# Kernel tuning notes

Measured on AMD Instinct MI355X. Metric: run time of the kernel, lower is better.

Reference implementation:

```python
import jax, jax.numpy as jnp
import numpy as np

B, C, CK, CV, W, H = 8, 256, 256, 256, 64, 64
EPS = 1e-6

def setup_inputs() -> dict:
    key = jax.random.key(0)
    ks = jax.random.split(key, 13)
    def wmat(k, shape, fan_in):
        return jax.random.normal(k, shape, jnp.float32) / np.float32(np.sqrt(fan_in))
    return {
        "x": jax.random.normal(ks[0], (B, C, W, H), jnp.float32),
        "qw": wmat(ks[1], (CK, C), C), "qb": jnp.zeros((CK,), jnp.float32),
        "kw": wmat(ks[2], (CK, C), C), "kb": jnp.zeros((CK,), jnp.float32),
        "vw": wmat(ks[3], (CV, C), C), "vb": jnp.zeros((CV,), jnp.float32),
        "rw": wmat(ks[4], (C, CV), CV), "rb": jnp.zeros((C,), jnp.float32),
        "c1w": wmat(ks[5], (C, C, 3, 3), C * 9), "c1b": jnp.zeros((C,), jnp.float32),
        "c2w": wmat(ks[6], (C, C, 3, 3), C * 9), "c2b": jnp.zeros((C,), jnp.float32),
    }

def reference(x, qw, qb, kw, kb, vw, vb, rw, rb, c1w, c1b, c2w, c2b):
    Bz, Cc, Wd, Hd = x.shape
    n = Wd * Hd
    xf = x.reshape(Bz, Cc, n)                                  # [b,c,n]
    Q = jnp.einsum('oc,bcn->bon', qw, xf) + qb[None, :, None]  # 1x1 conv
    K = jnp.einsum('oc,bcn->bon', kw, xf) + kb[None, :, None]
    V = jnp.einsum('oc,bcn->bon', vw, xf) + vb[None, :, None]
    # l2 norm over channel dim (per token), exactly as torch.norm(dim=-2)
    Qn = Q / jnp.linalg.norm(Q, axis=1, keepdims=True)
    Kn = K / jnp.linalg.norm(K, axis=1, keepdims=True)
    Qt = jnp.transpose(Qn, (0, 2, 1))                          # [b,n,ck]
    # head loops in the original sum over the full channel dim -> single einsum
    agg_dom = jnp.einsum('bnk,bk->bn', Qt, Kn.sum(-1))         # [b,n]
    denom = 1.0 / (n + agg_dom + EPS)                          # [b,n]
    vsum = V.sum(-1)                                           # [b,cv]
    kv = jnp.einsum('bkn,bcn->bkc', Kn, V)                     # K^T V, [b,ck,cv]
    qkv = jnp.einsum('bnk,bkc->bcn', Qt, kv)                   # [b,cv,n]
    wv = (vsum[:, :, None] + qkv) * denom[:, None, :]
    wv = wv.reshape(Bz, -1, Hd, Wd)                            # matches torch .view(b,cv,h,w)
    attn = jnp.einsum('oc,bchw->bohw', rw, wv) + rb[None, :, None, None]
    dn = ('NCHW', 'OIHW', 'NCHW')
    h = jax.lax.conv_general_dilated(attn, c1w, (1, 1), 'SAME', dimension_numbers=dn) + c1b[None, :, None, None]
    h = jax.lax.conv_general_dilated(h, c2w, (1, 1), 'SAME', dimension_numbers=dn) + c2b[None, :, None, None]
    return h * x + x
```

## Files before the change

### kernel.cpp

```cpp
#include <hip/hip_runtime.h>
#include <math.h>


typedef unsigned short u16;
typedef __attribute__((ext_vector_type(8))) short short8;
typedef __attribute__((ext_vector_type(4))) float f32x4;
typedef __attribute__((ext_vector_type(4))) unsigned short us4v;

#define ASYNC16(g, l) __builtin_amdgcn_global_load_lds( \
    (const __attribute__((address_space(1))) unsigned int*)(g), \
    (__attribute__((address_space(3))) unsigned int*)(l), 16, 0, 0)

static __device__ __forceinline__ float b2f(u16 h) {
  unsigned int u = ((unsigned int)h) << 16;
  return __builtin_bit_cast(float, u);
}
static __device__ __forceinline__ u16 f2b(float f) {
  unsigned int u = __builtin_bit_cast(unsigned int, f);
  u += 0x7fffu + ((u >> 16) & 1u);
  return (u16)(u >> 16);
}

#define NB 1048576L

__global__ __launch_bounds__(256) void prep1(
    const float* __restrict__ qw, const float* __restrict__ kw,
    const float* __restrict__ vw, const float* __restrict__ rw,
    const float* __restrict__ c1w, const float* __restrict__ c2w,
    const float* __restrict__ kb, const float* __restrict__ vb,
    const float* __restrict__ rb,
    u16* __restrict__ qw16, u16* __restrict__ kvw16, u16* __restrict__ rwT16,
    u16* __restrict__ wr1, u16* __restrict__ wr2,
    float* __restrict__ kvbias, float* __restrict__ zbuf, float* __restrict__ T)
{
  if (blockIdx.x >= 5633) {
    int m = blockIdx.x - 5633, co = threadIdx.x;
    float r = rb[co];
    const float* p = c1w + (long)m * 2304 + co * 9;
    float lv[9];
#pragma unroll
    for (int d = 0; d < 9; d++) lv[d] = p[d] * r;
#pragma unroll
    for (int d = 0; d < 9; d++)
#pragma unroll
      for (int off = 32; off; off >>= 1) lv[d] += __shfl_down(lv[d], off, 64);
    __shared__ float red[4][9];
    int w = co >> 6, l = co & 63;
    if (l == 0)
#pragma unroll
      for (int d = 0; d < 9; d++) red[w][d] = lv[d];
    __syncthreads();
    if (co < 9) T[m * 9 + co] = red[0][co] + red[1][co] + red[2][co] + red[3][co];
    return;
  }
  if (blockIdx.x == 5632) {
    int t = threadIdx.x;
    if (t < 256) { kvbias[t] = kb[t]; kvbias[t + 256] = vb[t]; }
    if (t < 64) zbuf[t] = 0.f;
    return;
  }
  long g = (long)blockIdx.x * 256 + threadIdx.x;
  if (g < 65536) {
    qw16[g] = f2b(qw[g]);
  } else if (g < 196608) {
    long e = g - 65536;
    kvw16[e] = f2b(e < 65536 ? kw[e] : vw[e - 65536]);
  } else if (g < 262144) {
    long e = g - 196608;
    int cv = e >> 8, co = e & 255;
    rwT16[e] = f2b(rw[co * 256 + cv]);
  } else if (g < 851968) {
    long e = g - 262144;
    int m = e / 2304, r = e - m * 2304;
    int d = r >> 8, c = r & 255;
    wr1[e] = f2b(c1w[m * 2304 + c * 9 + d]);
  } else {
    long e = g - 851968;
    int m = e / 2304, r = e - m * 2304;
    int d = r >> 8, c = r & 255;
    wr2[e] = f2b(c2w[m * 2304 + c * 9 + d]);
  }
}

__global__ __launch_bounds__(256) void transX(
    const float* __restrict__ x, u16* __restrict__ xT)
{
  __shared__ float Tl[64][65];
  int lin = blockIdx.x, t = threadIdx.x;
  int n0 = (lin & 63) * 64, c0 = ((lin >> 6) & 3) * 64, b = lin >> 8;
#pragma unroll
  for (int i = 0; i < 4; i++) {
    int c = (t >> 4) + i * 16, nn = (t & 15) * 4;
    float4 v = *(const float4*)&x[(long)b * NB + (long)(c0 + c) * 4096 + n0 + nn];
    Tl[c][nn] = v.x; Tl[c][nn + 1] = v.y; Tl[c][nn + 2] = v.z; Tl[c][nn + 3] = v.w;
  }
  __syncthreads();
#pragma unroll
  for (int i = 0; i < 4; i++) {
    int n = (t >> 4) + i * 16, cc = (t & 15) * 4;
    us4v o;
#pragma unroll
    for (int e = 0; e < 4; e++) o[e] = f2b(Tl[cc + e][n]);
    *(us4v*)&xT[(long)b * NB + (long)(n0 + n) * 256 + c0 + cc] = o;
  }
}

__global__ __launch_bounds__(256) void gemm3(
    const u16* __restrict__ wr1, const u16* __restrict__ rwT16, u16* __restrict__ w1p,
    const u16* __restrict__ xT, const u16* __restrict__ qw16, u16* __restrict__ Qt,
    const u16* __restrict__ kvw16, u16* __restrict__ KV,
    const float* __restrict__ qb, const float* __restrict__ kvbias,
    const float* __restrict__ T, const float* __restrict__ c1b,
    float* __restrict__ corr)
{
  __shared__ __align__(16) u16 As[2][128 * 32];
  __shared__ __align__(16) u16 Bs[2][128 * 32];
  int lin = blockIdx.x;
  if (lin >= 1572) {
    int e = (lin - 1572) * 256 + threadIdx.x;
    int m = e & 255, p = e >> 8;
    int y = p >> 6, xx = p & 63;
    float s = c1b[m];
#pragma unroll
    for (int d = 0; d < 9; d++) {
      int dy = d / 3 - 1, dx = d - (d / 3) * 3 - 1;
      if ((unsigned)(y + dy) < 64u && (unsigned)(xx + dx) < 64u) s += T[m * 9 + d];
    }
    corr[e] = s;
    return;
  }
  const u16 *A, *B;
  u16* out;
  const float *p1, *p2;
  long i0, j0, aoff, boff, ooff, sR;
  if (lin < 36) {
    int bx = lin & 1, by = lin >> 1;
    A = wr1; B = rwT16; out = w1p;
    i0 = by * 128; j0 = bx * 128;
    aoff = 0; boff = 0; ooff = 0; sR = 256;
    p1 = nullptr; p2 = nullptr;
  } else if (lin < 548) {
    int e = lin - 36;
    int bx = e & 1, by = (e >> 1) & 31, b = e >> 6;
    A = xT; B = qw16; out = Qt;
    i0 = by * 128; j0 = bx * 128;
    aoff = (long)b * NB; boff = 0; ooff = (long)b * NB; sR = 256;
    p1 = nullptr; p2 = qb;
  } else {
    int e = lin - 548;
    int bx = e & 31, by = (e >> 5) & 3, b = e >> 7;
    A = kvw16; B = xT; out = KV;
    i0 = by * 128; j0 = bx * 128;
    aoff = 0; boff = (long)b * NB; ooff = (long)b * 2 * NB; sR = 4096;
    p1 = kvbias; p2 = nullptr;
  }
  const u16* Ab = A + aoff + i0 * 256;
  const u16* Bb = B + boff + j0 * 256;
  int t = threadIdx.x, wave = t >> 6, lane = t & 63;
  int wi = (wave >> 1) * 64, wj = (wave & 1) * 64;
  int li = lane & 15, quad = lane >> 4;
  int qs = (lane & 3) ^ ((lane >> 3) & 3);
  int qx = quad ^ ((lane >> 1) & 3);
  int r0 = (wave * 128 + lane) >> 2;
  int r1 = (wave * 128 + 64 + lane) >> 2;
  f32x4 acc[4][4];
#pragma unroll
  for (int i = 0; i < 4; i++)
#pragma unroll
    for (int j = 0; j < 4; j++) acc[i][j] = (f32x4){0.f, 0.f, 0.f, 0.f};

  auto STAGE = [&](int kc, int buf) {
    int k0 = kc * 32;
    ASYNC16(Ab + (long)r0 * 256 + k0 + qs * 8, &As[buf][(wave * 128) * 8]);
    ASYNC16(Bb + (long)r0 * 256 + k0 + qs * 8, &Bs[buf][(wave * 128) * 8]);
    ASYNC16(Ab + (long)r1 * 256 + k0 + qs * 8, &As[buf][(wave * 128 + 64) * 8]);
    ASYNC16(Bb + (long)r1 * 256 + k0 + qs * 8, &Bs[buf][(wave * 128 + 64) * 8]);
  };

  int cur = 0;
  STAGE(0, 0);
#pragma unroll 1
  for (int kc = 0; kc < 8; kc++) {
    if (kc + 1 < 8) {
      STAGE(kc + 1, cur ^ 1);
      asm volatile("s_waitcnt vmcnt(4)" ::: "memory");
    } else {
      asm volatile("s_waitcnt vmcnt(0)" ::: "memory");
    }
    __builtin_amdgcn_s_barrier();
    const u16* as = &As[cur][0];
    const u16* bs = &Bs[cur][0];
    short8 af[4], bf[4];
#pragma unroll
    for (int s = 0; s < 4; s++) af[s] = *(const short8*)&as[(wi + s * 16 + li) * 32 + qx * 8];
#pragma unroll
    for (int s = 0; s < 4; s++) bf[s] = *(const short8*)&bs[(wj + s * 16 + li) * 32 + qx * 8];
#pragma unroll
    for (int si = 0; si < 4; si++)
#pragma unroll
      for (int sj = 0; sj < 4; sj++)
        acc[si][sj] = __builtin_amdgcn_mfma_f32_16x16x32_bf16(af[si], bf[sj], acc[si][sj], 0, 0, 0);
    __builtin_amdgcn_s_barrier();
    cur ^= 1;
  }

#pragma unroll
  for (int si = 0; si < 4; si++)
#pragma unroll
    for (int sj = 0; sj < 4; sj++) {
      long col = j0 + wj + sj * 16 + li;
#pragma unroll
      for (int r = 0; r < 4; r++) {
        long row = i0 + wi + si * 16 + quad * 4 + r;
        float v = acc[si][sj][r];
        if (p1) v += p1[row];
        if (p2) v += p2[col];
        out[ooff + row * sR + col] = f2b(v);
      }
    }
}

__global__ __launch_bounds__(256) void gemm_wv(
    const u16* __restrict__ Qt, const u16* __restrict__ kvT, u16* __restrict__ wvT,
    const float* __restrict__ vsum, const float* __restrict__ den,
    const float* __restrict__ rq)
{
  __shared__ __align__(16) u16 As[2][128 * 32];
  __shared__ __align__(16) u16 Bs[2][128 * 32];
  int lin = blockIdx.x;
  int bx = lin & 1, by = (lin >> 1) & 31, b = lin >> 6;
  long i0 = (long)by * 128;
  long j0 = (long)bx * 128;
  const u16* Ab = Qt + (long)b * NB + i0 * 256;
  const u16* Bb = kvT + (long)b * 65536 + j0 * 256;
  int t = threadIdx.x, wave = t >> 6, lane = t & 63;
  int wi = (wave >> 1) * 64, wj = (wave & 1) * 64;
  int li = lane & 15, quad = lane >> 4;
  int qs = (lane & 3) ^ ((lane >> 3) & 3);
  int qx = quad ^ ((lane >> 1) & 3);
  int r0 = (wave * 128 + lane) >> 2;
  int r1 = (wave * 128 + 64 + lane) >> 2;
  f32x4 acc[4][4];
#pragma unroll
  for (int i = 0; i < 4; i++)
#pragma unroll
    for (int j = 0; j < 4; j++) acc[i][j] = (f32x4){0.f, 0.f, 0.f, 0.f};

  auto STAGE = [&](int kc, int buf) {
    int k0 = kc * 32;
    ASYNC16(Ab + (long)r0 * 256 + k0 + qs * 8, &As[buf][(wave * 128) * 8]);
    ASYNC16(Bb + (long)r0 * 256 + k0 + qs * 8, &Bs[buf][(wave * 128) * 8]);
    ASYNC16(Ab + (long)r1 * 256 + k0 + qs * 8, &As[buf][(wave * 128 + 64) * 8]);
    ASYNC16(Bb + (long)r1 * 256 + k0 + qs * 8, &Bs[buf][(wave * 128 + 64) * 8]);
  };

  int cur = 0;
  STAGE(0, 0);
#pragma unroll 1
  for (int kc = 0; kc < 8; kc++) {
    if (kc + 1 < 8) {
      STAGE(kc + 1, cur ^ 1);
      asm volatile("s_waitcnt vmcnt(4)" ::: "memory");
    } else {
      asm volatile("s_waitcnt vmcnt(0)" ::: "memory");
    }
    __builtin_amdgcn_s_barrier();
    const u16* as = &As[cur][0];
    const u16* bs = &Bs[cur][0];
    short8 af[4], bf[4];
#pragma unroll
    for (int s = 0; s < 4; s++) af[s] = *(const short8*)&as[(wi + s * 16 + li) * 32 + qx * 8];
#pragma unroll
    for (int s = 0; s < 4; s++) bf[s] = *(const short8*)&bs[(wj + s * 16 + li) * 32 + qx * 8];
#pragma unroll
    for (int si = 0; si < 4; si++)
#pragma unroll
      for (int sj = 0; sj < 4; sj++)
        acc[si][sj] = __builtin_amdgcn_mfma_f32_16x16x32_bf16(af[si], bf[sj], acc[si][sj], 0, 0, 0);
    __builtin_amdgcn_s_barrier();
    cur ^= 1;
  }

#pragma unroll
  for (int si = 0; si < 4; si++)
#pragma unroll
    for (int sj = 0; sj < 4; sj++) {
      long col = j0 + wj + sj * 16 + li;
#pragma unroll
      for (int r = 0; r < 4; r++) {
        long row = i0 + wi + si * 16 + quad * 4 + r;
        float v = (acc[si][sj][r] * rq[b * 4096 + row] + vsum[b * 256 + col])
                  * den[b * 4096 + row];
        wvT[(long)b * NB + row * 256 + col] = f2b(v);
      }
    }
}

__global__ __launch_bounds__(256) void gemm_kv(
    const u16* __restrict__ KV, float* __restrict__ part)
{
  __shared__ __align__(16) u16 As[2][64 * 64];
  __shared__ __align__(16) u16 Bs[2][128 * 64];
  int z = blockIdx.z;
  int b = z & 7, sp = z >> 3;
  long i0 = (long)blockIdx.y * 64;
  long j0 = (long)blockIdx.x * 128;
  const u16* Ab = KV + (long)b * 2 * NB + i0 * 4096;
  const u16* Bb = KV + (long)b * 2 * NB + NB + j0 * 4096;
  int t = threadIdx.x, wave = t >> 6, lane = t & 63;
  int wm = (wave >> 1) * 32, wn = (wave & 1) * 64;
  int li = lane & 15, quad = lane >> 4;
  int qs8 = (lane & 7) ^ ((lane >> 3) & 7);
  int rr = wave * 8 + (lane >> 3);
  f32x4 acc[2][4];
#pragma unroll
  for (int i = 0; i < 2; i++)
#pragma unroll
    for (int j = 0; j < 4; j++) acc[i][j] = (f32x4){0.f, 0.f, 0.f, 0.f};

  auto STAGE = [&](int kc, int buf) {
    long k0 = (long)sp * 512 + kc * 64 + qs8 * 8;
    u16* ab = &As[buf][0];
    u16* bb = &Bs[buf][0];
    ASYNC16(Ab + (long)(rr)      * 4096 + k0, ab + wave * 512);
    ASYNC16(Ab + (long)(rr + 32) * 4096 + k0, ab + 2048 + wave * 512);
    ASYNC16(Bb + (long)(rr)      * 4096 + k0, bb + wave * 512);
    ASYNC16(Bb + (long)(rr + 32) * 4096 + k0, bb + 2048 + wave * 512);
    ASYNC16(Bb + (long)(rr + 64) * 4096 + k0, bb + 4096 + wave * 512);
    ASYNC16(Bb + (long)(rr + 96) * 4096 + k0, bb + 6144 + wave * 512);
  };

  int cur = 0;
  STAGE(0, 0);
#pragma unroll 1
  for (int kc = 0; kc < 8; kc++) {
    if (kc + 1 < 8) {
      STAGE(kc + 1, cur ^ 1);
      asm volatile("s_waitcnt vmcnt(6)" ::: "memory");
    } else {
      asm volatile("s_waitcnt vmcnt(0)" ::: "memory");
    }
    __builtin_amdgcn_s_barrier();
    const u16* as = &As[cur][0];
    const u16* bs = &Bs[cur][0];
#pragma unroll
    for (int kk = 0; kk < 2; kk++) {
      short8 af[2], bf[4];
      int slot = (((kk << 2) | quad) ^ (lane & 7)) * 8;
#pragma unroll
      for (int s = 0; s < 2; s++) af[s] = *(const short8*)&as[(wm + s * 16 + li) * 64 + slot];
#pragma unroll
      for (int s = 0; s < 4; s++) bf[s] = *(const short8*)&bs[(wn + s * 16 + li) * 64 + slot];
#pragma unroll
      for (int si = 0; si < 2; si++)
#pragma unroll
        for (int sj = 0; sj < 4; sj++)
          acc[si][sj] = __builtin_amdgcn_mfma_f32_16x16x32_bf16(af[si], bf[sj], acc[si][sj], 0, 0, 0);
    }
    __builtin_amdgcn_s_barrier();
    cur ^= 1;
  }

  float* outp = part + ((long)sp * 8 + b) * 65536;
#pragma unroll
  for (int si = 0; si < 2; si++)
#pragma unroll
    for (int sj = 0; sj < 4; sj++) {
      long col = j0 + wn + sj * 16 + li;
#pragma unroll
      for (int r = 0; r < 4; r++) {
        long row = i0 + wm + si * 16 + quad * 4 + r;
        outp[col * 256 + row] = acc[si][sj][r];
      }
    }
}

__global__ __launch_bounds__(256) void redkv_qden(
    const float* __restrict__ part, u16* __restrict__ kvT,
    const u16* __restrict__ Qt, const float* __restrict__ ksum,
    float* __restrict__ rq, float* __restrict__ den)
{
  int bb = blockIdx.x;
  if (bb < 2048) {
    int g = bb * 256 + threadIdx.x;
    float s = 0.f;
#pragma unroll
    for (int sp = 0; sp < 8; sp++) s += part[(long)sp * 524288 + g];
    kvT[g] = f2b(s);
    return;
  }
  int row = (bb - 2048) * 4 + (threadIdx.x >> 6);
  int lane = threadIdx.x & 63;
  int b = row >> 12;
  us4v v = *(const us4v*)(Qt + (long)row * 256 + lane * 4);
  float4 ks = *(const float4*)&ksum[b * 256 + lane * 4];
  float f0 = b2f(v[0]), f1 = b2f(v[1]), f2 = b2f(v[2]), f3 = b2f(v[3]);
  float s = f0 * f0 + f1 * f1 + f2 * f2 + f3 * f3;
  float s2 = f0 * ks.x + f1 * ks.y + f2 * ks.z + f3 * ks.w;
#pragma unroll
  for (int m = 32; m; m >>= 1) {
    s += __shfl_xor(s, m, 64);
    s2 += __shfl_xor(s2, m, 64);
  }
  if (lane == 0) {
    float r = 1.0f / sqrtf(s);
    rq[row] = r;
    den[row] = 1.0f / (4096.0f + s2 * r + 1e-6f);
  }
}

__global__ __launch_bounds__(256) void sumsqK(
    const u16* __restrict__ KV, float* __restrict__ rsqK)
{
  __shared__ float red[16][68];
  int b = blockIdx.x >> 6, nc = blockIdx.x & 63;
  int n0 = nc * 64;
  int t = threadIdx.x;
  int nn = (t & 15) * 4, cg = t >> 4;
  const u16* base = KV + (long)b * 2 * NB;
  float s0 = 0.f, s1 = 0.f, s2 = 0.f, s3 = 0.f;
  for (int st = 0; st < 16; st++) {
    int c = cg + st * 16;
    us4v v = *(const us4v*)(base + (long)c * 4096 + n0 + nn);
    float a = b2f(v[0]), bb = b2f(v[1]), cc = b2f(v[2]), dd = b2f(v[3]);
    s0 = fmaf(a, a, s0); s1 = fmaf(bb, bb, s1);
    s2 = fmaf(cc, cc, s2); s3 = fmaf(dd, dd, s3);
  }
  red[cg][nn] = s0; red[cg][nn + 1] = s1; red[cg][nn + 2] = s2; red[cg][nn + 3] = s3;
  __syncthreads();
  if (t < 64) {
    float s = 0.f;
#pragma unroll
    for (int g = 0; g < 16; g++) s += red[g][t];
    rsqK[b * 4096 + n0 + t] = 1.0f / sqrtf(s);
  }
}

__global__ __launch_bounds__(256) void scale_sums(
    u16* __restrict__ KV, const float* __restrict__ rsqK,
    float* __restrict__ ksum, float* __restrict__ vsum)
{
  int z = blockIdx.x;
  int isV = z >> 11, rem = z & 2047, b = rem >> 8, c = rem & 255;
  u16* row = KV + (long)b * 2 * NB + (long)isV * NB + (long)c * 4096;
  const float* rq = rsqK + b * 4096;
  int t = threadIdx.x;
  float s = 0.f;
  short8 v0 = *(const short8*)&row[t * 16];
  short8 v1 = *(const short8*)&row[t * 16 + 8];
  if (!isV) {
    short8 o0, o1;
#pragma unroll
    for (int e = 0; e < 8; e++) {
      float a = b2f((u16)v0[e]) * rq[t * 16 + e];
      float bb = b2f((u16)v1[e]) * rq[t * 16 + 8 + e];
      s += a + bb;
      o0[e] = (short)f2b(a); o1[e] = (short)f2b(bb);
    }
    *(short8*)&row[t * 16] = o0;
    *(short8*)&row[t * 16 + 8] = o1;
  } else {
#pragma unroll
    for (int e = 0; e < 8; e++) s += b2f((u16)v0[e]) + b2f((u16)v1[e]);
  }
#pragma unroll
  for (int off = 32; off; off >>= 1) s += __shfl_down(s, off, 64);
  __shared__ float red[4];
  if ((t & 63) == 0) red[t >> 6] = s;
  __syncthreads();
  if (t == 0)
    (isV ? vsum : ksum)[b * 256 + c] = red[0] + red[1] + red[2] + red[3];
}

__global__ __launch_bounds__(512, 2) void conv_gemm(
    const u16* __restrict__ inT, const u16* __restrict__ wr,
    const float* __restrict__ cb, const float* __restrict__ xres,
    const float* __restrict__ zbuf,
    u16* __restrict__ out16, float* __restrict__ out32, int mode)
{
  __shared__ __align__(16) u16 S[2 * 24576];

  int lin = blockIdx.x;
  int b   = lin & 7;
  int n0  = (lin >> 3) * 128;

  int t = threadIdx.x, wave = t >> 6, lane = t & 63;
  int wm = (wave >> 1) * 64, wn = (wave & 1) * 64;
  int li = lane & 15, quad = lane >> 4;
  int qs8 = (lane & 7) ^ ((lane >> 3) & 7);
  const u16* inb = inT + (long)b * NB;

  int rr = wave * 8 + (lane >> 3);
  const u16* Ap0 = wr + (long)(rr)       * 2304 + qs8 * 8;
  const u16* Ap1 = wr + (long)(rr + 64)  * 2304 + qs8 * 8;
  const u16* Ap2 = wr + (long)(rr + 128) * 2304 + qs8 * 8;
  const u16* Ap3 = wr + (long)(rr + 192) * 2304 + qs8 * 8;
  const u16* Bp0 = inb + (long)(n0 + rr) * 256 + qs8 * 8;
  const u16* Bp1 = inb + (long)(n0 + 64 + rr) * 256 + qs8 * 8;
  const u16* zp  = (const u16*)zbuf + qs8 * 8;
  int yb0 = n0 >> 6, xb = rr;

  f32x4 acc[4][4];
#pragma unroll
  for (int i = 0; i < 4; i++)
#pragma unroll
    for (int j = 0; j < 4; j++) acc[i][j] = (f32x4){0.f, 0.f, 0.f, 0.f};

  auto STAGE = [&](int ks, int buf) {
    int d = ks >> 2;
    int dy = d / 3 - 1, dx = d - (d / 3) * 3 - 1;
    long shA = (long)ks * 64;
    long shB = (long)(dy * 64 + dx) * 256 + (ks & 3) * 64;
    u16* base = &S[buf * 24576];
    ASYNC16(Ap0 + shA, base + wave * 512);
    ASYNC16(Ap1 + shA, base + 4096 + wave * 512);
    ASYNC16(Ap2 + shA, base + 8192 + wave * 512);
    ASYNC16(Ap3 + shA, base + 12288 + wave * 512);
    bool v0 = ((unsigned)(yb0 + dy) < 64u) && ((unsigned)(xb + dx) < 64u);
    bool v1 = ((unsigned)(yb0 + 1 + dy) < 64u) && ((unsigned)(xb + dx) < 64u);
    ASYNC16(v0 ? Bp0 + shB : zp, base + 16384 + wave * 512);
    ASYNC16(v1 ? Bp1 + shB : zp, base + 20480 + wave * 512);
  };

  int cur = 0;
  STAGE(0, 0);
#pragma unroll 1
  for (int ks = 0; ks < 36; ks++) {
    if (ks + 1 < 36) {
      STAGE(ks + 1, cur ^ 1);
      asm volatile("s_waitcnt vmcnt(6)" ::: "memory");
    } else {
      asm volatile("s_waitcnt vmcnt(0)" ::: "memory");
    }
    __builtin_amdgcn_s_barrier();
    const u16* as = &S[cur * 24576];
    const u16* bs = as + 16384;
#pragma unroll
    for (int kk = 0; kk < 2; kk++) {
      short8 af[4], bf[4];
      int slot = (((kk << 2) | quad) ^ (lane & 7)) * 8;
#pragma unroll
      for (int s = 0; s < 4; s++) af[s] = *(const short8*)&as[(wm + s * 16 + li) * 64 + slot];
#pragma unroll
      for (int s = 0; s < 4; s++) bf[s] = *(const short8*)&bs[(wn + s * 16 + li) * 64 + slot];
#pragma unroll
      for (int si = 0; si < 4; si++)
#pragma unroll
        for (int sj = 0; sj < 4; sj++)
          acc[si][sj] = __builtin_amdgcn_mfma_f32_16x16x32_bf16(af[si], bf[sj], acc[si][sj], 0, 0, 0);
    }
    __builtin_amdgcn_s_barrier();
    cur ^= 1;
  }

#pragma unroll
  for (int si = 0; si < 4; si++)
#pragma unroll
    for (int sj = 0; sj < 4; sj++) {
      int n = n0 + wn + sj * 16 + li;
      int m0 = wm + si * 16 + quad * 4;
      if (mode == 0) {
        f32x4 c4 = *(const f32x4*)&cb[(long)n * 256 + m0];
        us4v o;
#pragma unroll
        for (int r = 0; r < 4; r++) o[r] = f2b(acc[si][sj][r] + c4[r]);
        *(us4v*)&out16[(long)b * NB + (long)n * 256 + m0] = o;
      } else {
#pragma unroll
        for (int r = 0; r < 4; r++) {
          int m = m0 + r;
          float v = acc[si][sj][r] + cb[m];
          long a = (long)b * NB + (long)m * 4096 + n;
          float xv = xres[a];
          out32[a] = fmaf(v, xv, xv);
        }
      }
    }
}

extern "C" void kernel_launch(void* const* d_in, const int* in_sizes, int n_in,
                              void* d_out, int out_size, void* d_ws, size_t ws_size,
                              hipStream_t stream)
{
  const float* x   = (const float*)d_in[0];
  const float* qw  = (const float*)d_in[1];
  const float* qb  = (const float*)d_in[2];
  const float* kw  = (const float*)d_in[3];
  const float* kb  = (const float*)d_in[4];
  const float* vw  = (const float*)d_in[5];
  const float* vb  = (const float*)d_in[6];
  const float* rw  = (const float*)d_in[7];
  const float* rb  = (const float*)d_in[8];
  const float* c1w = (const float*)d_in[9];
  const float* c1b = (const float*)d_in[10];
  const float* c2w = (const float*)d_in[11];
  const float* c2b = (const float*)d_in[12];

  u16* U     = (u16*)d_ws;
  u16* xT16  = U;
  u16* Qt16  = U + 8388608;
  u16* KV16  = U + 16777216;
  u16* wr2   = U + 33554432;
  u16* kvT16 = U + 34144256;
  float* Fws = (float*)(U + 34668544);
  float* ksum = Fws;
  float* vsum = Fws + 2048;
  float* zbuf = Fws + 4096;

  char* ob = (char*)d_out;
  float* kvpart = (float*)(ob + 0);
  float* den    = (float*)(ob + 16777216);
  float* rsqK   = (float*)(ob + 16908288);
  float* corr   = (float*)(ob + 17039360);
  u16*   w1p16  = (u16*)(ob + 21233664);
  u16*   wr1    = (u16*)(ob + 22413312);
  float* T      = (float*)(ob + 23592960);
  u16*   rwT16  = (u16*)(ob + 23629824);
  u16*   qw16   = (u16*)(ob + 23760896);
  u16*   kvw16  = (u16*)(ob + 23891968);
  float* kvbias = (float*)(ob + 24154112);
  float* rq     = (float*)(ob + 24158208);
  float* outF   = (float*)d_out;

  u16* wvT16 = xT16;
  u16* h1T16 = Qt16;

  dim3 blk(256);

  prep1<<<5889, blk, 0, stream>>>(qw, kw, vw, rw, c1w, c2w, kb, vb, rb,
                                  qw16, kvw16, rwT16, wr1, wr2, kvbias, zbuf, T);
  transX<<<2048, blk, 0, stream>>>(x, xT16);

  gemm3<<<5668, blk, 0, stream>>>(wr1, rwT16, w1p16, xT16, qw16, Qt16,
                                  kvw16, KV16, qb, kvbias, T, c1b, corr);

  sumsqK<<<512, blk, 0, stream>>>(KV16, rsqK);
  scale_sums<<<4096, blk, 0, stream>>>(KV16, rsqK, ksum, vsum);

  gemm_kv<<<dim3(2, 4, 64), blk, 0, stream>>>(KV16, kvpart);
  redkv_qden<<<10240, blk, 0, stream>>>(kvpart, kvT16, Qt16, ksum, rq, den);

  gemm_wv<<<512, blk, 0, stream>>>(Qt16, kvT16, wvT16, vsum, den, rq);

  conv_gemm<<<256, 512, 0, stream>>>(wvT16, w1p16, corr, nullptr, zbuf,
                                     h1T16, nullptr, 0);
  conv_gemm<<<256, 512, 0, stream>>>(h1T16, wr2, c2b, x, zbuf,
                                     nullptr, outF, 1);
}
```

Before: 309.3 us.

## Fuse K norm and V sums into GEMM epilogue, merge transpose into prep

Folds the x transpose into the prep kernel, which now also zeroes the accumulators. The K/V projection GEMM epilogue now computes per-token K squared norms and per-channel V sums with atomics. This removes the separate sumsqK kernel and the V half of scale_sums, leaving a K-only scaleK pass that computes rsqrt inline. gemm_kv is retiled to 64x64 output tiles with more blocks. The change cuts two launches and a full re-read of KV, at the cost of float atomics and nondeterministic summation order.

```diff
diff --git a/kernel.cpp b/kernel.cpp
--- a/kernel.cpp
+++ b/kernel.cpp
@@ -31,10 +31,43 @@
     const float* __restrict__ rb,
     u16* __restrict__ qw16, u16* __restrict__ kvw16, u16* __restrict__ rwT16,
     u16* __restrict__ wr1, u16* __restrict__ wr2,
-    float* __restrict__ kvbias, float* __restrict__ zbuf, float* __restrict__ T)
-{
-  if (blockIdx.x >= 5633) {
-    int m = blockIdx.x - 5633, co = threadIdx.x;
+    float* __restrict__ kvbias, float* __restrict__ zbuf, float* __restrict__ T,
+    const float* __restrict__ x, u16* __restrict__ xT,
+    float* __restrict__ colsq, float* __restrict__ vsum)
+{
+  __shared__ float Tl[64][65];
+  int bb = blockIdx.x, t = threadIdx.x;
+  if (bb >= 8065) {
+    int idx = (bb - 8065) * 256 + t;
+    vsum[idx] = 0.f;
+    return;
+  }
+  if (bb >= 7937) {
+    colsq[(bb - 7937) * 256 + t] = 0.f;
+    return;
+  }
+  if (bb >= 5889) {
+    int lin = bb - 5889;
+    int n0 = (lin & 63) * 64, c0 = ((lin >> 6) & 3) * 64, b = lin >> 8;
+#pragma unroll
+    for (int i = 0; i < 4; i++) {
+      int c = (t >> 4) + i * 16, nn = (t & 15) * 4;
+      float4 v = *(const float4*)&x[(long)b * NB + (long)(c0 + c) * 4096 + n0 + nn];
+      Tl[c][nn] = v.x; Tl[c][nn + 1] = v.y; Tl[c][nn + 2] = v.z; Tl[c][nn + 3] = v.w;
+    }
+    __syncthreads();
+#pragma unroll
+    for (int i = 0; i < 4; i++) {
+      int n = (t >> 4) + i * 16, cc = (t & 15) * 4;
+      us4v o;
+#pragma unroll
+      for (int e = 0; e < 4; e++) o[e] = f2b(Tl[cc + e][n]);
+      *(us4v*)&xT[(long)b * NB + (long)(n0 + n) * 256 + c0 + cc] = o;
+    }
+    return;
+  }
+  if (bb >= 5633) {
+    int m = bb - 5633, co = t;
     float r = rb[co];
     const float* p = c1w + (long)m * 2304 + co * 9;
     float lv[9];
@@ -53,13 +86,12 @@
     if (co < 9) T[m * 9 + co] = red[0][co] + red[1][co] + red[2][co] + red[3][co];
     return;
   }
-  if (blockIdx.x == 5632) {
-    int t = threadIdx.x;
+  if (bb == 5632) {
     if (t < 256) { kvbias[t] = kb[t]; kvbias[t + 256] = vb[t]; }
     if (t < 64) zbuf[t] = 0.f;
     return;
   }
-  long g = (long)blockIdx.x * 256 + threadIdx.x;
+  long g = (long)bb * 256 + t;
   if (g < 65536) {
     qw16[g] = f2b(qw[g]);
   } else if (g < 196608) {
@@ -82,36 +114,14 @@
   }
 }
 
-__global__ __launch_bounds__(256) void transX(
-    const float* __restrict__ x, u16* __restrict__ xT)
-{
-  __shared__ float Tl[64][65];
-  int lin = blockIdx.x, t = threadIdx.x;
-  int n0 = (lin & 63) * 64, c0 = ((lin >> 6) & 3) * 64, b = lin >> 8;
-#pragma unroll
-  for (int i = 0; i < 4; i++) {
-    int c = (t >> 4) + i * 16, nn = (t & 15) * 4;
-    float4 v = *(const float4*)&x[(long)b * NB + (long)(c0 + c) * 4096 + n0 + nn];
-    Tl[c][nn] = v.x; Tl[c][nn + 1] = v.y; Tl[c][nn + 2] = v.z; Tl[c][nn + 3] = v.w;
-  }
-  __syncthreads();
-#pragma unroll
-  for (int i = 0; i < 4; i++) {
-    int n = (t >> 4) + i * 16, cc = (t & 15) * 4;
-    us4v o;
-#pragma unroll
-    for (int e = 0; e < 4; e++) o[e] = f2b(Tl[cc + e][n]);
-    *(us4v*)&xT[(long)b * NB + (long)(n0 + n) * 256 + c0 + cc] = o;
-  }
-}
-
 __global__ __launch_bounds__(256) void gemm3(
     const u16* __restrict__ wr1, const u16* __restrict__ rwT16, u16* __restrict__ w1p,
     const u16* __restrict__ xT, const u16* __restrict__ qw16, u16* __restrict__ Qt,
     const u16* __restrict__ kvw16, u16* __restrict__ KV,
     const float* __restrict__ qb, const float* __restrict__ kvbias,
     const float* __restrict__ T, const float* __restrict__ c1b,
-    float* __restrict__ corr)
+    float* __restrict__ corr,
+    float* __restrict__ colsq, float* __restrict__ vsum)
 {
   __shared__ __align__(16) u16 As[2][128 * 32];
   __shared__ __align__(16) u16 Bs[2][128 * 32];
@@ -133,26 +143,27 @@
   u16* out;
   const float *p1, *p2;
   long i0, j0, aoff, boff, ooff, sR;
+  int job, bz = 0;
   if (lin < 36) {
     int bx = lin & 1, by = lin >> 1;
     A = wr1; B = rwT16; out = w1p;
     i0 = by * 128; j0 = bx * 128;
     aoff = 0; boff = 0; ooff = 0; sR = 256;
-    p1 = nullptr; p2 = nullptr;
+    p1 = nullptr; p2 = nullptr; job = 0;
   } else if (lin < 548) {
     int e = lin - 36;
     int bx = e & 1, by = (e >> 1) & 31, b = e >> 6;
     A = xT; B = qw16; out = Qt;
     i0 = by * 128; j0 = bx * 128;
     aoff = (long)b * NB; boff = 0; ooff = (long)b * NB; sR = 256;
-    p1 = nullptr; p2 = qb;
+    p1 = nullptr; p2 = qb; job = 1; bz = b;
   } else {
     int e = lin - 548;
     int bx = e & 31, by = (e >> 5) & 3, b = e >> 7;
     A = kvw16; B = xT; out = KV;
     i0 = by * 128; j0 = bx * 128;
     aoff = 0; boff = (long)b * NB; ooff = (long)b * 2 * NB; sR = 4096;
-    p1 = kvbias; p2 = nullptr;
+    p1 = kvbias; p2 = nullptr; job = 2; bz = b;
   }
   const u16* Ab = A + aoff + i0 * 256;
   const u16* Bb = B + boff + j0 * 256;
@@ -218,6 +229,179 @@
         out[ooff + row * sR + col] = f2b(v);
       }
     }
+
+  if (job == 2) {
+    if (i0 < 256) {
+#pragma unroll
+      for (int sj = 0; sj < 4; sj++) {
+        long col = j0 + wj + sj * 16 + li;
+        float c2 = 0.f;
+#pragma unroll
+        for (int si = 0; si < 4; si++)
+#pragma unroll
+          for (int r = 0; r < 4; r++) {
+            float v = acc[si][sj][r] + p1[i0 + wi + si * 16 + quad * 4 + r];
+            c2 = fmaf(v, v, c2);
+          }
+        c2 += __shfl_xor(c2, 16, 64);
+        c2 += __shfl_xor(c2, 32, 64);
+        if (quad == 0) atomicAdd(&colsq[bz * 4096 + col], c2);
+      }
+    } else {
+#pragma unroll
+      for (int si = 0; si < 4; si++)
+#pragma unroll
+        for (int r = 0; r < 4; r++) {
+          long row = i0 + wi + si * 16 + quad * 4 + r;
+          float p = acc[si][0][r] + acc[si][1][r] + acc[si][2][r] + acc[si][3][r]
+                    + 4.0f * p1[row];
+#pragma unroll
+          for (int m = 1; m < 16; m <<= 1) p += __shfl_xor(p, m, 64);
+          if (li == 0) atomicAdd(&vsum[bz * 256 + (row - 256)], p);
+        }
+    }
+  }
+}
+
+__global__ __launch_bounds__(256) void scaleK(
+    u16* __restrict__ KV, const float* __restrict__ colsq, float* __restrict__ ksum)
+{
+  int z = blockIdx.x;
+  int b = z >> 8, c = z & 255;
+  u16* row = KV + (long)b * 2 * NB + (long)c * 4096;
+  const float* cs = colsq + b * 4096;
+  int t = threadIdx.x;
+  float s = 0.f;
+  short8 v0 = *(const short8*)&row[t * 16];
+  short8 v1 = *(const short8*)&row[t * 16 + 8];
+  short8 o0, o1;
+#pragma unroll
+  for (int e = 0; e < 8; e++) {
+    float q0 = 1.0f / sqrtf(cs[t * 16 + e]);
+    float q1 = 1.0f / sqrtf(cs[t * 16 + 8 + e]);
+    float a = b2f((u16)v0[e]) * q0;
+    float bb = b2f((u16)v1[e]) * q1;
+    s += a + bb;
+    o0[e] = (short)f2b(a); o1[e] = (short)f2b(bb);
+  }
+  *(short8*)&row[t * 16] = o0;
+  *(short8*)&row[t * 16 + 8] = o1;
+#pragma unroll
+  for (int off = 32; off; off >>= 1) s += __shfl_down(s, off, 64);
+  __shared__ float red[4];
+  if ((t & 63) == 0) red[t >> 6] = s;
+  __syncthreads();
+  if (t == 0) ksum[b * 256 + c] = red[0] + red[1] + red[2] + red[3];
+}
+
+__global__ __launch_bounds__(256) void gemm_kv(
+    const u16* __restrict__ KV, float* __restrict__ part)
+{
+  __shared__ __align__(16) u16 As[2][64 * 64];
+  __shared__ __align__(16) u16 Bs[2][64 * 64];
+  int z = blockIdx.z;
+  int b = z & 7, sp = z >> 3;
+  long i0 = (long)blockIdx.y * 64;
+  long j0 = (long)blockIdx.x * 64;
+  const u16* Ab = KV + (long)b * 2 * NB + i0 * 4096;
+  const u16* Bb = KV + (long)b * 2 * NB + NB + j0 * 4096;
+  int t = threadIdx.x, wave = t >> 6, lane = t & 63;
+  int wm = (wave >> 1) * 32, wn = (wave & 1) * 32;
+  int li = lane & 15, quad = lane >> 4;
+  int qs8 = (lane & 7) ^ ((lane >> 3) & 7);
+  f32x4 acc[2][2];
+#pragma unroll
+  for (int i = 0; i < 2; i++)
+#pragma unroll
+    for (int j = 0; j < 2; j++) acc[i][j] = (f32x4){0.f, 0.f, 0.f, 0.f};
+
+  auto STAGE = [&](int kc, int buf) {
+    long k0 = (long)sp * 512 + kc * 64 + qs8 * 8;
+#pragma unroll
+    for (int j = 0; j < 2; j++) {
+      int row = (wave * 2 + j) * 8 + (lane >> 3);
+      ASYNC16(Ab + (long)row * 4096 + k0, &As[buf][(wave * 2 + j) * 512]);
+      ASYNC16(Bb + (long)row * 4096 + k0, &Bs[buf][(wave * 2 + j) * 512]);
+    }
+  };
+
+  int cur = 0;
+  STAGE(0, 0);
+#pragma unroll 1
+  for (int kc = 0; kc < 8; kc++) {
+    if (kc + 1 < 8) {
+      STAGE(kc + 1, cur ^ 1);
+      asm volatile("s_waitcnt vmcnt(4)" ::: "memory");
+    } else {
+      asm volatile("s_waitcnt vmcnt(0)" ::: "memory");
+    }
+    __builtin_amdgcn_s_barrier();
+    const u16* as = &As[cur][0];
+    const u16* bs = &Bs[cur][0];
+#pragma unroll
+    for (int kk = 0; kk < 2; kk++) {
+      short8 af[2], bf[2];
+      int slot = (((kk << 2) | quad) ^ (lane & 7)) * 8;
+#pragma unroll
+      for (int s = 0; s < 2; s++) af[s] = *(const short8*)&as[(wm + s * 16 + li) * 64 + slot];
+#pragma unroll
+      for (int s = 0; s < 2; s++) bf[s] = *(const short8*)&bs[(wn + s * 16 + li) * 64 + slot];
+#pragma unroll
+      for (int si = 0; si < 2; si++)
+#pragma unroll
+        for (int sj = 0; sj < 2; sj++)
+          acc[si][sj] = __builtin_amdgcn_mfma_f32_16x16x32_bf16(af[si], bf[sj], acc[si][sj], 0, 0, 0);
+    }
+    __builtin_amdgcn_s_barrier();
+    cur ^= 1;
+  }
+
+  float* outp = part + ((long)sp * 8 + b) * 65536;
+#pragma unroll
+  for (int si = 0; si < 2; si++)
+#pragma unroll
+    for (int sj = 0; sj < 2; sj++) {
+      long col = j0 + wn + sj * 16 + li;
+#pragma unroll
+      for (int r = 0; r < 4; r++) {
+        long row = i0 + wm + si * 16 + quad * 4 + r;
+        outp[col * 256 + row] = acc[si][sj][r];
+      }
+    }
+}
+
+__global__ __launch_bounds__(256) void redkv_qden(
+    const float* __restrict__ part, u16* __restrict__ kvT,
+    const u16* __restrict__ Qt, const float* __restrict__ ksum,
+    float* __restrict__ rq, float* __restrict__ den)
+{
+  int bb = blockIdx.x;
+  if (bb < 2048) {
+    int g = bb * 256 + threadIdx.x;
+    float s = 0.f;
+#pragma unroll
+    for (int sp = 0; sp < 8; sp++) s += part[(long)sp * 524288 + g];
+    kvT[g] = f2b(s);
+    return;
+  }
+  int row = (bb - 2048) * 4 + (threadIdx.x >> 6);
+  int lane = threadIdx.x & 63;
+  int b = row >> 12;
+  us4v v = *(const us4v*)(Qt + (long)row * 256 + lane * 4);
+  float4 ks = *(const float4*)&ksum[b * 256 + lane * 4];
+  float f0 = b2f(v[0]), f1 = b2f(v[1]), f2 = b2f(v[2]), f3 = b2f(v[3]);
+  float s = f0 * f0 + f1 * f1 + f2 * f2 + f3 * f3;
+  float s2 = f0 * ks.x + f1 * ks.y + f2 * ks.z + f3 * ks.w;
+#pragma unroll
+  for (int m = 32; m; m >>= 1) {
+    s += __shfl_xor(s, m, 64);
+    s2 += __shfl_xor(s2, m, 64);
+  }
+  if (lane == 0) {
+    float r = 1.0f / sqrtf(s);
+    rq[row] = r;
+    den[row] = 1.0f / (4096.0f + s2 * r + 1e-6f);
+  }
 }
 
 __global__ __launch_bounds__(256) void gemm_wv(
@@ -296,182 +480,6 @@
     }
 }
 
-__global__ __launch_bounds__(256) void gemm_kv(
-    const u16* __restrict__ KV, float* __restrict__ part)
-{
-  __shared__ __align__(16) u16 As[2][64 * 64];
-  __shared__ __align__(16) u16 Bs[2][128 * 64];
-  int z = blockIdx.z;
-  int b = z & 7, sp = z >> 3;
-  long i0 = (long)blockIdx.y * 64;
-  long j0 = (long)blockIdx.x * 128;
-  const u16* Ab = KV + (long)b * 2 * NB + i0 * 4096;
-  const u16* Bb = KV + (long)b * 2 * NB + NB + j0 * 4096;
-  int t = threadIdx.x, wave = t >> 6, lane = t & 63;
-  int wm = (wave >> 1) * 32, wn = (wave & 1) * 64;
-  int li = lane & 15, quad = lane >> 4;
-  int qs8 = (lane & 7) ^ ((lane >> 3) & 7);
-  int rr = wave * 8 + (lane >> 3);
-  f32x4 acc[2][4];
-#pragma unroll
-  for (int i = 0; i < 2; i++)
-#pragma unroll
-    for (int j = 0; j < 4; j++) acc[i][j] = (f32x4){0.f, 0.f, 0.f, 0.f};
-
-  auto STAGE = [&](int kc, int buf) {
-    long k0 = (long)sp * 512 + kc * 64 + qs8 * 8;
-    u16* ab = &As[buf][0];
-    u16* bb = &Bs[buf][0];
-    ASYNC16(Ab + (long)(rr)      * 4096 + k0, ab + wave * 512);
-    ASYNC16(Ab + (long)(rr + 32) * 4096 + k0, ab + 2048 + wave * 512);
-    ASYNC16(Bb + (long)(rr)      * 4096 + k0, bb + wave * 512);
-    ASYNC16(Bb + (long)(rr + 32) * 4096 + k0, bb + 2048 + wave * 512);
-    ASYNC16(Bb + (long)(rr + 64) * 4096 + k0, bb + 4096 + wave * 512);
-    ASYNC16(Bb + (long)(rr + 96) * 4096 + k0, bb + 6144 + wave * 512);
-  };
-
-  int cur = 0;
-  STAGE(0, 0);
-#pragma unroll 1
-  for (int kc = 0; kc < 8; kc++) {
-    if (kc + 1 < 8) {
-      STAGE(kc + 1, cur ^ 1);
-      asm volatile("s_waitcnt vmcnt(6)" ::: "memory");
-    } else {
-      asm volatile("s_waitcnt vmcnt(0)" ::: "memory");
-    }
-    __builtin_amdgcn_s_barrier();
-    const u16* as = &As[cur][0];
-    const u16* bs = &Bs[cur][0];
-#pragma unroll
-    for (int kk = 0; kk < 2; kk++) {
-      short8 af[2], bf[4];
-      int slot = (((kk << 2) | quad) ^ (lane & 7)) * 8;
-#pragma unroll
-      for (int s = 0; s < 2; s++) af[s] = *(const short8*)&as[(wm + s * 16 + li) * 64 + slot];
-#pragma unroll
-      for (int s = 0; s < 4; s++) bf[s] = *(const short8*)&bs[(wn + s * 16 + li) * 64 + slot];
-#pragma unroll
-      for (int si = 0; si < 2; si++)
-#pragma unroll
-        for (int sj = 0; sj < 4; sj++)
-          acc[si][sj] = __builtin_amdgcn_mfma_f32_16x16x32_bf16(af[si], bf[sj], acc[si][sj], 0, 0, 0);
-    }
-    __builtin_amdgcn_s_barrier();
-    cur ^= 1;
-  }
-
-  float* outp = part + ((long)sp * 8 + b) * 65536;
-#pragma unroll
-  for (int si = 0; si < 2; si++)
-#pragma unroll
-    for (int sj = 0; sj < 4; sj++) {
-      long col = j0 + wn + sj * 16 + li;
-#pragma unroll
-      for (int r = 0; r < 4; r++) {
-        long row = i0 + wm + si * 16 + quad * 4 + r;
-        outp[col * 256 + row] = acc[si][sj][r];
-      }
-    }
-}
-
-__global__ __launch_bounds__(256) void redkv_qden(
-    const float* __restrict__ part, u16* __restrict__ kvT,
-    const u16* __restrict__ Qt, const float* __restrict__ ksum,
-    float* __restrict__ rq, float* __restrict__ den)
-{
-  int bb = blockIdx.x;
-  if (bb < 2048) {
-    int g = bb * 256 + threadIdx.x;
-    float s = 0.f;
-#pragma unroll
-    for (int sp = 0; sp < 8; sp++) s += part[(long)sp * 524288 + g];
-    kvT[g] = f2b(s);
-    return;
-  }
-  int row = (bb - 2048) * 4 + (threadIdx.x >> 6);
-  int lane = threadIdx.x & 63;
-  int b = row >> 12;
-  us4v v = *(const us4v*)(Qt + (long)row * 256 + lane * 4);
-  float4 ks = *(const float4*)&ksum[b * 256 + lane * 4];
-  float f0 = b2f(v[0]), f1 = b2f(v[1]), f2 = b2f(v[2]), f3 = b2f(v[3]);
-  float s = f0 * f0 + f1 * f1 + f2 * f2 + f3 * f3;
-  float s2 = f0 * ks.x + f1 * ks.y + f2 * ks.z + f3 * ks.w;
-#pragma unroll
-  for (int m = 32; m; m >>= 1) {
-    s += __shfl_xor(s, m, 64);
-    s2 += __shfl_xor(s2, m, 64);
-  }
-  if (lane == 0) {
-    float r = 1.0f / sqrtf(s);
-    rq[row] = r;
-    den[row] = 1.0f / (4096.0f + s2 * r + 1e-6f);
-  }
-}
-
-__global__ __launch_bounds__(256) void sumsqK(
-    const u16* __restrict__ KV, float* __restrict__ rsqK)
-{
-  __shared__ float red[16][68];
-  int b = blockIdx.x >> 6, nc = blockIdx.x & 63;
-  int n0 = nc * 64;
-  int t = threadIdx.x;
-  int nn = (t & 15) * 4, cg = t >> 4;
-  const u16* base = KV + (long)b * 2 * NB;
-  float s0 = 0.f, s1 = 0.f, s2 = 0.f, s3 = 0.f;
-  for (int st = 0; st < 16; st++) {
-    int c = cg + st * 16;
-    us4v v = *(const us4v*)(base + (long)c * 4096 + n0 + nn);
-    float a = b2f(v[0]), bb = b2f(v[1]), cc = b2f(v[2]), dd = b2f(v[3]);
-    s0 = fmaf(a, a, s0); s1 = fmaf(bb, bb, s1);
-    s2 = fmaf(cc, cc, s2); s3 = fmaf(dd, dd, s3);
-  }
-  red[cg][nn] = s0; red[cg][nn + 1] = s1; red[cg][nn + 2] = s2; red[cg][nn + 3] = s3;
-  __syncthreads();
-  if (t < 64) {
-    float s = 0.f;
-#pragma unroll
-    for (int g = 0; g < 16; g++) s += red[g][t];
-    rsqK[b * 4096 + n0 + t] = 1.0f / sqrtf(s);
-  }
-}
-
-__global__ __launch_bounds__(256) void scale_sums(
-    u16* __restrict__ KV, const float* __restrict__ rsqK,
-    float* __restrict__ ksum, float* __restrict__ vsum)
-{
-  int z = blockIdx.x;
-  int isV = z >> 11, rem = z & 2047, b = rem >> 8, c = rem & 255;
-  u16* row = KV + (long)b * 2 * NB + (long)isV * NB + (long)c * 4096;
-  const float* rq = rsqK + b * 4096;
-  int t = threadIdx.x;
-  float s = 0.f;
-  short8 v0 = *(const short8*)&row[t * 16];
-  short8 v1 = *(const short8*)&row[t * 16 + 8];
-  if (!isV) {
-    short8 o0, o1;
-#pragma unroll
-    for (int e = 0; e < 8; e++) {
-      float a = b2f((u16)v0[e]) * rq[t * 16 + e];
-      float bb = b2f((u16)v1[e]) * rq[t * 16 + 8 + e];
-      s += a + bb;
-      o0[e] = (short)f2b(a); o1[e] = (short)f2b(bb);
-    }
-    *(short8*)&row[t * 16] = o0;
-    *(short8*)&row[t * 16 + 8] = o1;
-  } else {
-#pragma unroll
-    for (int e = 0; e < 8; e++) s += b2f((u16)v0[e]) + b2f((u16)v1[e]);
-  }
-#pragma unroll
-  for (int off = 32; off; off >>= 1) s += __shfl_down(s, off, 64);
-  __shared__ float red[4];
-  if ((t & 63) == 0) red[t >> 6] = s;
-  __syncthreads();
-  if (t == 0)
-    (isV ? vsum : ksum)[b * 256 + c] = red[0] + red[1] + red[2] + red[3];
-}
-
 __global__ __launch_bounds__(512, 2) void conv_gemm(
     const u16* __restrict__ inT, const u16* __restrict__ wr,
     const float* __restrict__ cb, const float* __restrict__ xres,
@@ -610,7 +618,7 @@
   char* ob = (char*)d_out;
   float* kvpart = (float*)(ob + 0);
   float* den    = (float*)(ob + 16777216);
-  float* rsqK   = (float*)(ob + 16908288);
+  float* colsq  = (float*)(ob + 16908288);
   float* corr   = (float*)(ob + 17039360);
   u16*   w1p16  = (u16*)(ob + 21233664);
   u16*   wr1    = (u16*)(ob + 22413312);
@@ -627,17 +635,17 @@
 
   dim3 blk(256);
 
-  prep1<<<5889, blk, 0, stream>>>(qw, kw, vw, rw, c1w, c2w, kb, vb, rb,
-                                  qw16, kvw16, rwT16, wr1, wr2, kvbias, zbuf, T);
-  transX<<<2048, blk, 0, stream>>>(x, xT16);
+  prep1<<<8073, blk, 0, stream>>>(qw, kw, vw, rw, c1w, c2w, kb, vb, rb,
+                                  qw16, kvw16, rwT16, wr1, wr2, kvbias, zbuf, T,
+                                  x, xT16, colsq, vsum);
 
   gemm3<<<5668, blk, 0, stream>>>(wr1, rwT16, w1p16, xT16, qw16, Qt16,
-                                  kvw16, KV16, qb, kvbias, T, c1b, corr);
-
-  sumsqK<<<512, blk, 0, stream>>>(KV16, rsqK);
-  scale_sums<<<4096, blk, 0, stream>>>(KV16, rsqK, ksum, vsum);
-
-  gemm_kv<<<dim3(2, 4, 64), blk, 0, stream>>>(KV16, kvpart);
+                                  kvw16, KV16, qb, kvbias, T, c1b, corr,
+                                  colsq, vsum);
+
+  scaleK<<<2048, blk, 0, stream>>>(KV16, colsq, ksum);
+
+  gemm_kv<<<dim3(4, 4, 64), blk, 0, stream>>>(KV16, kvpart);
   redkv_qden<<<10240, blk, 0, stream>>>(kvpart, kvT16, Qt16, ksum, rq, den);
 
   gemm_wv<<<512, blk, 0, stream>>>(Qt16, kvT16, wvT16, vsum, den, rq);
```

Result: slower. 318.4 us (+3.0%).
